# Optimization experiments

Measured on AMD Instinct MI355X. Metric: run time of the kernel, lower is better.

The kernel has to match this reference:

```python
import jax, jax.numpy as jnp
import numpy as np

MASS = 0.5
G = 1.0  # constant offset -p[8]*g in the objective; does not affect argmin u*
NEWTON_ITERS = 30


def _lambertw(x):
    """Solve w*exp(w) = x for x >= 0 (principal branch) via Newton iterations."""
    w = jnp.log1p(x)  # good init on [0, inf)
    for _ in range(NEWTON_ITERS):
        ew = jnp.exp(w)
        w = w - (w * ew - x) / (ew * (w + 1.0))
    return w


def setup_inputs() -> dict:
    key = jax.random.key(0)
    kz, kt, k1, k2 = jax.random.split(key, 4)
    B, S, H = 500000, 12, 100
    return {
        "z": jax.random.normal(kz, (B, S), jnp.float32),
        "t": jax.random.uniform(kt, (B,), jnp.float32),
        "W1": jax.random.normal(k1, (S + 1, H), jnp.float32) * 0.1,
        "b1": jnp.zeros((H,), jnp.float32),
        "W2": jax.random.normal(k2, (H, S), jnp.float32) * 0.1,
        "b2": jnp.zeros((S,), jnp.float32),
    }


def reference(z, t, W1, b1, W2, b2):
    # p_net: MLP on concat([t, z])
    inp = jnp.concatenate([t[:, None], z], axis=1)          # [B, 13]
    h = jnp.tanh(inp @ W1 + b1)                              # [B, 100]
    p = h @ W2 + b2                                          # [B, 12]
    # Objective: c . u + exp(0.5*||u||^2) + const, with
    # c = [(p6+p7+p8)/m, p9, p10, p11]. Stationarity: c + u*exp(0.5||u||^2)=0
    # => u = -c*exp(-0.5*w), where w = ||u||^2 solves w*e^w = ||c||^2 (Lambert W).
    c = jnp.stack(
        [(p[:, 6] + p[:, 7] + p[:, 8]) / MASS, p[:, 9], p[:, 10], p[:, 11]],
        axis=1,
    )                                                        # [B, 4]
    x = jnp.sum(c * c, axis=1)                               # [B] = ||c||^2
    w = _lambertw(x)                                         # [B]
    ustar = -c * jnp.exp(-0.5 * w)[:, None]                  # [B, 4]
    return ustar
```

## Files before the change

### kernel.cpp

```cpp
#include <hip/hip_runtime.h>


constexpr int S = 12;
constexpr int H = 100;
#define TWO_LOG2E 2.8853900817779268f

typedef _Float16 h2 __attribute__((ext_vector_type(2)));

__device__ __forceinline__ float fast_rcp(float x) {
    return __builtin_amdgcn_rcpf(x);
}

__device__ __forceinline__ h2 bit_h2(unsigned int u) {
    union { unsigned int u; h2 h; } cv; cv.u = u; return cv.h;
}

#if __has_builtin(__builtin_amdgcn_fdot2)
__device__ __forceinline__ float fdot2(h2 a, h2 b, float c) {
    return __builtin_amdgcn_fdot2(a, b, c, false);
}
#else
__device__ __forceinline__ float fdot2(h2 a, h2 b, float c) {
    return fmaf((float)a.x, (float)b.x, fmaf((float)a.y, (float)b.y, c));
}
#endif

__device__ __forceinline__ h2 pk16(float a, float b) {
#if __has_builtin(__builtin_amdgcn_cvt_pkrtz)
    union {
        __fp16 __attribute__((ext_vector_type(2))) f;
        h2 h;
    } cv;
    cv.f = __builtin_amdgcn_cvt_pkrtz(a, b);
    return cv.h;
#else
    h2 r; r.x = (_Float16)a; r.y = (_Float16)b; return r;
#endif
}

__global__ __launch_bounds__(256) void pack_weights(
    const float* __restrict__ W1, const float* __restrict__ b1,
    const float* __restrict__ W2, unsigned int* __restrict__ ws)
{
    int idx = blockIdx.x * 256 + threadIdx.x;
    if (idx < 800) {
        int jp = idx >> 4, s = idx & 15;
        unsigned int v;
        if (s < 14) {
            int unit = 2 * jp + (s >= 7);
            int q = (s < 7) ? s : s - 7;
            int k0 = 2 * q, k1 = 2 * q + 1;
            float w0 = W1[k0 * H + unit] * TWO_LOG2E;
            float w1 = (k1 < 13) ? W1[k1 * H + unit] * TWO_LOG2E : 0.0f;
            union { h2 h; unsigned int u; } cv;
            cv.h = pk16(w0, w1);
            v = cv.u;
        } else {
            int unit = 2 * jp + (s - 14);
            union { float f; unsigned int u; } cv;
            cv.f = b1[unit] * TWO_LOG2E;
            v = cv.u;
        }
        ws[idx] = v;
    } else if (idx < 1200) {
        int r = idx - 800;
        int jp = r >> 3, m = r & 7;
        unsigned int v = 0;
        if (m < 6) {
            float w0 = W2[(2 * jp) * S + 6 + m];
            float w1 = W2[(2 * jp + 1) * S + 6 + m];
            union { h2 h; unsigned int u; } cv;
            cv.h = pk16(w0, w1);
            v = cv.u;
        }
        ws[idx] = v;
    }
}

__global__ __launch_bounds__(256) void cvx_quad_kernel(
    const float* __restrict__ z, const float* __restrict__ t,
    const unsigned int* __restrict__ ws, const float* __restrict__ b2,
    float* __restrict__ out, int B)
{
    int tid = blockIdx.x * 256 + threadIdx.x;
    int i0 = tid * 2;
    if (i0 >= B) return;
    int i1 = (i0 + 1 < B) ? (i0 + 1) : (B - 1);

    h2 inA[7], inB[7];
    {
        const float4* zr0 = reinterpret_cast<const float4*>(z) + (size_t)i0 * 3;
        const float4* zr1 = reinterpret_cast<const float4*>(z) + (size_t)i1 * 3;
        float4 a0 = zr0[0], a1 = zr0[1], a2 = zr0[2];
        float4 d0 = zr1[0], d1 = zr1[1], d2 = zr1[2];
        inA[0] = pk16(t[i0], a0.x);
        inA[1] = pk16(a0.y, a0.z);
        inA[2] = pk16(a0.w, a1.x);
        inA[3] = pk16(a1.y, a1.z);
        inA[4] = pk16(a1.w, a2.x);
        inA[5] = pk16(a2.y, a2.z);
        inA[6] = pk16(a2.w, 0.0f);
        inB[0] = pk16(t[i1], d0.x);
        inB[1] = pk16(d0.y, d0.z);
        inB[2] = pk16(d0.w, d1.x);
        inB[3] = pk16(d1.y, d1.z);
        inB[4] = pk16(d1.w, d2.x);
        inB[5] = pk16(d2.y, d2.z);
        inB[6] = pk16(d2.w, 0.0f);
    }

    float pA[6], pB[6];
    #pragma unroll
    for (int m = 0; m < 6; ++m) {
        float bm = b2[6 + m];
        pA[m] = bm;
        pB[m] = bm;
    }

    #pragma unroll 2
    for (int jp = 0; jp < H / 2; ++jp) {
        const unsigned int* ra = ws + jp * 16;
        const unsigned int* rb = ws + 800 + jp * 8;

        float fb0 = __uint_as_float(ra[14]);
        float fb1 = __uint_as_float(ra[15]);
        float accA0 = fb0, accA1 = fb1, accB0 = fb0, accB1 = fb1;
        #pragma unroll
        for (int q = 0; q < 7; ++q) {
            h2 w0 = bit_h2(ra[q]);
            h2 w1 = bit_h2(ra[7 + q]);
            accA0 = fdot2(inA[q], w0, accA0);
            accA1 = fdot2(inA[q], w1, accA1);
            accB0 = fdot2(inB[q], w0, accB0);
            accB1 = fdot2(inB[q], w1, accB1);
        }

        float aA0 = 1.0f + __builtin_amdgcn_exp2f(accA0);
        float aA1 = 1.0f + __builtin_amdgcn_exp2f(accA1);
        float aB0 = 1.0f + __builtin_amdgcn_exp2f(accB0);
        float aB1 = 1.0f + __builtin_amdgcn_exp2f(accB1);
        float sA = -2.0f * fast_rcp(aA0 * aA1);
        float sB = -2.0f * fast_rcp(aB0 * aB1);
        float thA0 = fmaf(aA1, sA, 1.0f);
        float thA1 = fmaf(aA0, sA, 1.0f);
        float thB0 = fmaf(aB1, sB, 1.0f);
        float thB1 = fmaf(aB0, sB, 1.0f);
        h2 tA = pk16(thA0, thA1);
        h2 tB = pk16(thB0, thB1);

        #pragma unroll
        for (int m = 0; m < 6; ++m) {
            h2 qm = bit_h2(rb[m]);
            pA[m] = fdot2(tA, qm, pA[m]);
            pB[m] = fdot2(tB, qm, pB[m]);
        }
    }

    #pragma unroll
    for (int e = 0; e < 2; ++e) {
        const float* p = e ? pB : pA;
        float c0 = 2.0f * (p[0] + p[1] + p[2]);
        float c1 = p[3], c2 = p[4], c3 = p[5];
        float x = fmaf(c0, c0, fmaf(c1, c1, fmaf(c2, c2, c3 * c3)));

        float w = __logf(1.0f + x);
        #pragma unroll
        for (int it = 0; it < 5; ++it) {
            float ew  = __expf(w);
            float num = fmaf(w, ew, -x);
            float den = fmaf(ew, w, ew);
            w = w - num * fast_rcp(den);
        }

        float sc = -__expf(-0.5f * w);
        float4 o;
        o.x = c0 * sc;
        o.y = c1 * sc;
        o.z = c2 * sc;
        o.w = c3 * sc;
        reinterpret_cast<float4*>(out)[e ? i1 : i0] = o;
    }
}

extern "C" void kernel_launch(void* const* d_in, const int* in_sizes, int n_in,
                              void* d_out, int out_size, void* d_ws, size_t ws_size,
                              hipStream_t stream) {
    const float* z  = (const float*)d_in[0];
    const float* t  = (const float*)d_in[1];
    const float* W1 = (const float*)d_in[2];
    const float* b1 = (const float*)d_in[3];
    const float* W2 = (const float*)d_in[4];
    const float* b2 = (const float*)d_in[5];
    float* out = (float*)d_out;
    unsigned int* ws = (unsigned int*)d_ws;

    pack_weights<<<dim3(5), dim3(256), 0, stream>>>(W1, b1, W2, ws);

    int B = in_sizes[1];
    int threads = (B + 1) / 2;
    int grid = (threads + 255) / 256;
    cvx_quad_kernel<<<dim3(grid), dim3(256), 0, stream>>>(z, t, ws, b2, out, B);
}
```

Before: 104.8 us.

## Process one row per thread and software-prefetch packed weights as uint4

Drops the two-rows-per-thread layout so each thread handles a single sample, doubling the thread count. Weights are now read as uint4 vectors and the next hidden pair's weights are prefetched into registers one iteration ahead. The packed weight buffer gains a zero-padded extra slot so the final prefetch stays in bounds. This gives up the reuse of each weight load across two samples in exchange for more parallelism and lower register pressure, which may raise occupancy, at the cost of doubling the per-sample weight load traffic.

After: 104.8 us. About the same (+0.0%).

```diff
diff --git a/kernel.cpp b/kernel.cpp
--- a/kernel.cpp
+++ b/kernel.cpp
@@ -4,6 +4,7 @@
 constexpr int S = 12;
 constexpr int H = 100;
 #define TWO_LOG2E 2.8853900817779268f
+#define REG_B 816
 
 typedef _Float16 h2 __attribute__((ext_vector_type(2)));
 
@@ -43,30 +44,32 @@
     const float* __restrict__ W2, unsigned int* __restrict__ ws)
 {
     int idx = blockIdx.x * 256 + threadIdx.x;
-    if (idx < 800) {
+    if (idx < REG_B) {
         int jp = idx >> 4, s = idx & 15;
-        unsigned int v;
-        if (s < 14) {
-            int unit = 2 * jp + (s >= 7);
-            int q = (s < 7) ? s : s - 7;
-            int k0 = 2 * q, k1 = 2 * q + 1;
-            float w0 = W1[k0 * H + unit] * TWO_LOG2E;
-            float w1 = (k1 < 13) ? W1[k1 * H + unit] * TWO_LOG2E : 0.0f;
-            union { h2 h; unsigned int u; } cv;
-            cv.h = pk16(w0, w1);
-            v = cv.u;
-        } else {
-            int unit = 2 * jp + (s - 14);
-            union { float f; unsigned int u; } cv;
-            cv.f = b1[unit] * TWO_LOG2E;
-            v = cv.u;
+        unsigned int v = 0;
+        if (jp < 50) {
+            if (s < 14) {
+                int unit = 2 * jp + (s >= 7);
+                int q = (s < 7) ? s : s - 7;
+                int k0 = 2 * q, k1 = 2 * q + 1;
+                float w0 = W1[k0 * H + unit] * TWO_LOG2E;
+                float w1 = (k1 < 13) ? W1[k1 * H + unit] * TWO_LOG2E : 0.0f;
+                union { h2 h; unsigned int u; } cv;
+                cv.h = pk16(w0, w1);
+                v = cv.u;
+            } else {
+                int unit = 2 * jp + (s - 14);
+                union { float f; unsigned int u; } cv;
+                cv.f = b1[unit] * TWO_LOG2E;
+                v = cv.u;
+            }
         }
         ws[idx] = v;
-    } else if (idx < 1200) {
-        int r = idx - 800;
+    } else if (idx < REG_B + 408) {
+        int r = idx - REG_B;
         int jp = r >> 3, m = r & 7;
         unsigned int v = 0;
-        if (m < 6) {
+        if (jp < 50 && m < 6) {
             float w0 = W2[(2 * jp) * S + 6 + m];
             float w1 = W2[(2 * jp + 1) * S + 6 + m];
             union { h2 h; unsigned int u; } cv;
@@ -82,104 +85,96 @@
     const unsigned int* __restrict__ ws, const float* __restrict__ b2,
     float* __restrict__ out, int B)
 {
-    int tid = blockIdx.x * 256 + threadIdx.x;
-    int i0 = tid * 2;
-    if (i0 >= B) return;
-    int i1 = (i0 + 1 < B) ? (i0 + 1) : (B - 1);
+    int i = blockIdx.x * 256 + threadIdx.x;
+    if (i >= B) return;
 
-    h2 inA[7], inB[7];
+    h2 in[7];
     {
-        const float4* zr0 = reinterpret_cast<const float4*>(z) + (size_t)i0 * 3;
-        const float4* zr1 = reinterpret_cast<const float4*>(z) + (size_t)i1 * 3;
-        float4 a0 = zr0[0], a1 = zr0[1], a2 = zr0[2];
-        float4 d0 = zr1[0], d1 = zr1[1], d2 = zr1[2];
-        inA[0] = pk16(t[i0], a0.x);
-        inA[1] = pk16(a0.y, a0.z);
-        inA[2] = pk16(a0.w, a1.x);
-        inA[3] = pk16(a1.y, a1.z);
-        inA[4] = pk16(a1.w, a2.x);
-        inA[5] = pk16(a2.y, a2.z);
-        inA[6] = pk16(a2.w, 0.0f);
-        inB[0] = pk16(t[i1], d0.x);
-        inB[1] = pk16(d0.y, d0.z);
-        inB[2] = pk16(d0.w, d1.x);
-        inB[3] = pk16(d1.y, d1.z);
-        inB[4] = pk16(d1.w, d2.x);
-        inB[5] = pk16(d2.y, d2.z);
-        inB[6] = pk16(d2.w, 0.0f);
+        const float4* zr = reinterpret_cast<const float4*>(z) + (size_t)i * 3;
+        float4 a0 = zr[0], a1 = zr[1], a2 = zr[2];
+        in[0] = pk16(t[i], a0.x);
+        in[1] = pk16(a0.y, a0.z);
+        in[2] = pk16(a0.w, a1.x);
+        in[3] = pk16(a1.y, a1.z);
+        in[4] = pk16(a1.w, a2.x);
+        in[5] = pk16(a2.y, a2.z);
+        in[6] = pk16(a2.w, 0.0f);
     }
 
-    float pA[6], pB[6];
+    float p[6];
     #pragma unroll
-    for (int m = 0; m < 6; ++m) {
-        float bm = b2[6 + m];
-        pA[m] = bm;
-        pB[m] = bm;
-    }
+    for (int m = 0; m < 6; ++m) p[m] = b2[6 + m];
+
+    const uint4* A4 = reinterpret_cast<const uint4*>(ws);
+    const uint4* B4 = reinterpret_cast<const uint4*>(ws + REG_B);
+
+    uint4 a0 = A4[0], a1 = A4[1], a2 = A4[2], a3 = A4[3];
+    uint4 r0 = B4[0], r1 = B4[1];
 
     #pragma unroll 2
     for (int jp = 0; jp < H / 2; ++jp) {
-        const unsigned int* ra = ws + jp * 16;
-        const unsigned int* rb = ws + 800 + jp * 8;
+        uint4 na0 = A4[(jp + 1) * 4 + 0];
+        uint4 na1 = A4[(jp + 1) * 4 + 1];
+        uint4 na2 = A4[(jp + 1) * 4 + 2];
+        uint4 na3 = A4[(jp + 1) * 4 + 3];
+        uint4 nr0 = B4[(jp + 1) * 2 + 0];
+        uint4 nr1 = B4[(jp + 1) * 2 + 1];
 
-        float fb0 = __uint_as_float(ra[14]);
-        float fb1 = __uint_as_float(ra[15]);
-        float accA0 = fb0, accA1 = fb1, accB0 = fb0, accB1 = fb1;
-        #pragma unroll
-        for (int q = 0; q < 7; ++q) {
-            h2 w0 = bit_h2(ra[q]);
-            h2 w1 = bit_h2(ra[7 + q]);
-            accA0 = fdot2(inA[q], w0, accA0);
-            accA1 = fdot2(inA[q], w1, accA1);
-            accB0 = fdot2(inB[q], w0, accB0);
-            accB1 = fdot2(inB[q], w1, accB1);
-        }
+        float acc0 = __uint_as_float(a3.z);
+        float acc1 = __uint_as_float(a3.w);
+        acc0 = fdot2(in[0], bit_h2(a0.x), acc0);
+        acc0 = fdot2(in[1], bit_h2(a0.y), acc0);
+        acc0 = fdot2(in[2], bit_h2(a0.z), acc0);
+        acc0 = fdot2(in[3], bit_h2(a0.w), acc0);
+        acc0 = fdot2(in[4], bit_h2(a1.x), acc0);
+        acc0 = fdot2(in[5], bit_h2(a1.y), acc0);
+        acc0 = fdot2(in[6], bit_h2(a1.z), acc0);
+        acc1 = fdot2(in[0], bit_h2(a1.w), acc1);
+        acc1 = fdot2(in[1], bit_h2(a2.x), acc1);
+        acc1 = fdot2(in[2], bit_h2(a2.y), acc1);
+        acc1 = fdot2(in[3], bit_h2(a2.z), acc1);
+        acc1 = fdot2(in[4], bit_h2(a2.w), acc1);
+        acc1 = fdot2(in[5], bit_h2(a3.x), acc1);
+        acc1 = fdot2(in[6], bit_h2(a3.y), acc1);
 
-        float aA0 = 1.0f + __builtin_amdgcn_exp2f(accA0);
-        float aA1 = 1.0f + __builtin_amdgcn_exp2f(accA1);
-        float aB0 = 1.0f + __builtin_amdgcn_exp2f(accB0);
-        float aB1 = 1.0f + __builtin_amdgcn_exp2f(accB1);
-        float sA = -2.0f * fast_rcp(aA0 * aA1);
-        float sB = -2.0f * fast_rcp(aB0 * aB1);
-        float thA0 = fmaf(aA1, sA, 1.0f);
-        float thA1 = fmaf(aA0, sA, 1.0f);
-        float thB0 = fmaf(aB1, sB, 1.0f);
-        float thB1 = fmaf(aB0, sB, 1.0f);
-        h2 tA = pk16(thA0, thA1);
-        h2 tB = pk16(thB0, thB1);
+        float e0 = 1.0f + __builtin_amdgcn_exp2f(acc0);
+        float e1 = 1.0f + __builtin_amdgcn_exp2f(acc1);
+        float s  = -2.0f * fast_rcp(e0 * e1);
+        float th0 = fmaf(e1, s, 1.0f);
+        float th1 = fmaf(e0, s, 1.0f);
+        h2 th = pk16(th0, th1);
 
-        #pragma unroll
-        for (int m = 0; m < 6; ++m) {
-            h2 qm = bit_h2(rb[m]);
-            pA[m] = fdot2(tA, qm, pA[m]);
-            pB[m] = fdot2(tB, qm, pB[m]);
-        }
+        p[0] = fdot2(th, bit_h2(r0.x), p[0]);
+        p[1] = fdot2(th, bit_h2(r0.y), p[1]);
+        p[2] = fdot2(th, bit_h2(r0.z), p[2]);
+        p[3] = fdot2(th, bit_h2(r0.w), p[3]);
+        p[4] = fdot2(th, bit_h2(r1.x), p[4]);
+        p[5] = fdot2(th, bit_h2(r1.y), p[5]);
+
+        a0 = na0; a1 = na1; a2 = na2; a3 = na3;
+        r0 = nr0; r1 = nr1;
     }
 
+    float c0 = 2.0f * (p[0] + p[1] + p[2]);
+    float c1 = p[3], c2 = p[4], c3 = p[5];
+    float x = fmaf(c0, c0, fmaf(c1, c1, fmaf(c2, c2, c3 * c3)));
+
+    float w = __logf(1.0f + x);
     #pragma unroll
-    for (int e = 0; e < 2; ++e) {
-        const float* p = e ? pB : pA;
-        float c0 = 2.0f * (p[0] + p[1] + p[2]);
-        float c1 = p[3], c2 = p[4], c3 = p[5];
-        float x = fmaf(c0, c0, fmaf(c1, c1, fmaf(c2, c2, c3 * c3)));
+    for (int it = 0; it < 5; ++it) {
+        float ew  = __expf(w);
+        float num = fmaf(w, ew, -x);
+        float den = fmaf(ew, w, ew);
+        w = w - num * fast_rcp(den);
+    }
 
-        float w = __logf(1.0f + x);
-        #pragma unroll
-        for (int it = 0; it < 5; ++it) {
-            float ew  = __expf(w);
-            float num = fmaf(w, ew, -x);
-            float den = fmaf(ew, w, ew);
-            w = w - num * fast_rcp(den);
-        }
-
-        float sc = -__expf(-0.5f * w);
-        float4 o;
-        o.x = c0 * sc;
-        o.y = c1 * sc;
-        o.z = c2 * sc;
-        o.w = c3 * sc;
-        reinterpret_cast<float4*>(out)[e ? i1 : i0] = o;
-    }
+    float sc = -__expf(-0.5f * w);
+    float4 o;
+    o.x = c0 * sc;
+    o.y = c1 * sc;
+    o.z = c2 * sc;
+    o.w = c3 * sc;
+    reinterpret_cast<float4*>(out)[i] = o;
 }
 
 extern "C" void kernel_launch(void* const* d_in, const int* in_sizes, int n_in,
@@ -197,7 +192,6 @@
     pack_weights<<<dim3(5), dim3(256), 0, stream>>>(W1, b1, W2, ws);
 
     int B = in_sizes[1];
-    int threads = (B + 1) / 2;
-    int grid = (threads + 255) / 256;
+    int grid = (B + 255) / 256;
     cvx_quad_kernel<<<dim3(grid), dim3(256), 0, stream>>>(z, t, ws, b2, out, B);
 }
```
